# Performance work log

Measured on AMD Instinct MI355X. Metric: run time of the kernel, lower is better.

The kernel has to match this reference:

```python
import jax, jax.numpy as jnp
import numpy as np

# Straight-through sign binarization: forward -> {-1, +1}, backward -> identity
@jax.custom_vjp
def binarize(x):
    return jnp.where(x >= 0, jnp.ones_like(x), -jnp.ones_like(x))

def _bin_fwd(x):
    return binarize(x), None

def _bin_bwd(res, g):
    return (g,)

binarize.defvjp(_bin_fwd, _bin_bwd)

BATCH = 16384
IN_SIZE = 1025   # must be 2**n + 1
HIDDEN = 1025    # must be 2**n + 1

def setup_inputs() -> dict:
    key = jax.random.key(0)
    k0, k1, k2, k3 = jax.random.split(key, 4)
    # weight init scale per reset_parameters: sqrt(1.5/(in+out)) uniform
    s = float(np.sqrt(1.5 / (IN_SIZE + HIDDEN)))
    return {
        "x": jax.random.normal(k0, (BATCH, IN_SIZE), dtype=jnp.float32),
        "W0": jax.random.uniform(k1, (HIDDEN, IN_SIZE), jnp.float32, -s, s),
        "W1": jax.random.uniform(k2, (HIDDEN, HIDDEN), jnp.float32, -s, s),
        "W2": jax.random.uniform(k3, (1, HIDDEN), jnp.float32, -s, s),
    }

def reference(x, W0, W1, W2):
    # x: [B, IN_SIZE]; weights stored [out, in] (nn.Linear convention), no bias
    h = x.reshape(-1, IN_SIZE)
    for W in (W0, W1, W2):
        lin = h @ binarize(W).T          # float GEMM against +/-1 weights
        h = binarize(lin)                # sign activation
    # num_classes == 2 path: to_boolean maps {-1,+1} -> {0,1}, then squeeze
    out = (h + 1.0) * 0.5
    return out.squeeze(-1)               # [B]
```

## Files before the change

kernel.cpp:

```cpp
#include <hip/hip_runtime.h>
#include <cstdint>

typedef unsigned long long u64;
typedef unsigned short ushort_t;
typedef __attribute__((ext_vector_type(8))) short short8;
typedef __attribute__((ext_vector_type(4))) float f32x4;

#define B_TOTAL 16384
#define K_DIM   1025
#define O_DIM   1025
#define NWORDS  17
#define NKT     34
#define NFRAG   72
#define A_BYTES 8192
#define B_BYTES 73728
#define STEP_BYTES (A_BYTES + B_BYTES)
#define FLAG_CAP 4096

__device__ __forceinline__ ushort_t f2bf_rne(float f) {
  unsigned u = __float_as_uint(f);
  return (ushort_t)((u + 0x7fffu + ((u >> 16) & 1u)) >> 16);
}

__device__ __forceinline__ void gload16(const ushort_t* g, char* l) {
  __builtin_amdgcn_global_load_lds(
      (const __attribute__((address_space(1))) void*)g,
      (__attribute__((address_space(3))) void*)l, 16, 0, 0);
}

__global__ __launch_bounds__(256) void pack_all_kernel(const float* __restrict__ W0,
                                                       const float* __restrict__ W1,
                                                       const float* __restrict__ W2,
                                                       u64* __restrict__ w0b,
                                                       u64* __restrict__ w1b,
                                                       u64* __restrict__ w2b) {
  __shared__ unsigned char by[136];
  const int row = blockIdx.x, t = threadIdx.x;
  const float* src; u64* dst; int o;
  if (row < O_DIM)           { src = W0; dst = w0b; o = row; }
  else if (row < 2 * O_DIM)  { src = W1; dst = w1b; o = row - O_DIM; }
  else                       { src = W2; dst = w2b; o = 0; }
  if (t < 136) {
    const float* wr = src + (size_t)o * K_DIM;
    unsigned m = 0;
#pragma unroll
    for (int j = 0; j < 8; ++j) {
      int k = t * 8 + j;
      bool pos = (k < K_DIM) ? (wr[k] >= 0.0f) : true;
      m |= (unsigned)pos << j;
    }
    by[t] = (unsigned char)m;
  }
  __syncthreads();
  if (t < NWORDS) {
    u64 word = 0;
#pragma unroll
    for (int q = 0; q < 8; ++q) word |= (u64)by[t * 8 + q] << (8 * q);
    dst[(size_t)o * NWORDS + t] = word;
  }
}

__global__ __launch_bounds__(256) void prep_sbf_kernel(const float* __restrict__ w0,
                                                       ushort_t* __restrict__ sbf) {
  const int t = threadIdx.x;
  const int f = blockIdx.x * 4 + (t >> 6);
  const int lane = t & 63;
  const int kt = f / NFRAG, nf = f % NFRAG;
  const int o = nf * 16 + (lane & 15);
  const int kbase = kt * 32 + (lane >> 4) * 8;
  short8 sv;
#pragma unroll
  for (int j = 0; j < 8; ++j) {
    int k = kbase + j;
    short v = 0;
    if (o < O_DIM && k < K_DIM)
      v = (short)((w0[(size_t)o * K_DIM + k] >= 0.0f) ? 0x3F80 : 0xBF80);
    sv[j] = v;
  }
  *(short8*)&sbf[(size_t)f * 512 + lane * 8] = sv;
}

__global__ __launch_bounds__(256) void prep_xf_kernel(const float* __restrict__ x,
                                                      ushort_t* __restrict__ xf,
                                                      float* __restrict__ errb) {
  const int p = blockIdx.x, t = threadIdx.x;
  const int mf = t >> 6, lane = t & 63;
  const int lr = lane & 15, lg = lane >> 4;
  const int brow = p * 64 + mf * 16 + lr;
  const float* xr = x + (size_t)brow * K_DIM;
  float s = 0.0f;
  for (int kt = 0; kt < NKT; ++kt) {
    const int kbase = kt * 32 + lg * 8;
    float v[8];
    if (kbase + 8 <= K_DIM) {
      float4 a = *(const float4*)(xr + kbase);
      float4 b = *(const float4*)(xr + kbase + 4);
      v[0]=a.x; v[1]=a.y; v[2]=a.z; v[3]=a.w; v[4]=b.x; v[5]=b.y; v[6]=b.z; v[7]=b.w;
    } else {
#pragma unroll
      for (int j = 0; j < 8; ++j) v[j] = (kbase + j < K_DIM) ? xr[kbase + j] : 0.0f;
    }
    short8 hi, lo;
#pragma unroll
    for (int j = 0; j < 8; ++j) {
      s += fabsf(v[j]);
      ushort_t h = f2bf_rne(v[j]);
      float hf = __uint_as_float((unsigned)h << 16);
      ushort_t l = f2bf_rne(v[j] - hf);
      hi[j] = (short)h; lo[j] = (short)l;
    }
    size_t base = ((size_t)(p * NKT + kt) * 8 + mf) * 512 + lane * 8;
    *(short8*)&xf[base] = hi;
    *(short8*)&xf[base + 4 * 512] = lo;
  }
  s += __shfl_xor(s, 16, 64);
  s += __shfl_xor(s, 32, 64);
  if (lg == 0) errb[brow] = s * (1.02f / 65536.0f) + 0.125f;
}

__global__ __launch_bounds__(512, 2) void l1_fused_kernel(
    const ushort_t* __restrict__ xf, const ushort_t* __restrict__ sbf,
    const float* __restrict__ errb, const float* __restrict__ x,
    const u64* __restrict__ w0b, const u64* __restrict__ w1b,
    const u64* __restrict__ w2b, float* __restrict__ out) {
  extern __shared__ char smem[];
  const int p = blockIdx.x;
  const int t = threadIdx.x;
  const int wave = t >> 6, lane = t & 63;
  const int lr = lane & 15, lg = lane >> 4;
  const int b0 = p * 64;
  const int obase = wave * 144;

  const ushort_t* gA = xf + (size_t)p * NKT * (A_BYTES / 2);

  f32x4 acc[4][9];
#pragma unroll
  for (int mf = 0; mf < 4; ++mf)
#pragma unroll
    for (int nfl = 0; nfl < 9; ++nfl)
#pragma unroll
      for (int c = 0; c < 4; ++c) acc[mf][nfl][c] = 0.0f;

#define STAGE(BUFI, KT)                                                        \
  {                                                                            \
    char* dbuf = smem + (BUFI) * STEP_BYTES;                                   \
    _Pragma("unroll")                                                          \
    for (int i = 0; i < 10; ++i) {                                             \
      int s = wave * 10 + i;                                                   \
      const ushort_t* g = (s < 8)                                              \
          ? gA + (KT) * (A_BYTES / 2) + s * 512 + lane * 8                     \
          : sbf + (size_t)(KT) * (B_BYTES / 2) + (s - 8) * 512 + lane * 8;     \
      gload16(g, dbuf + s * 1024);                                             \
    }                                                                          \
  }

  STAGE(0, 0);
  __syncthreads();
  int cur = 0;
  for (int kt = 0; kt < NKT; ++kt) {
    if (kt + 1 < NKT) STAGE(cur ^ 1, kt + 1);
    const ushort_t* A = (const ushort_t*)(smem + cur * STEP_BYTES);
    const ushort_t* Bf = A + A_BYTES / 2;
    short8 ah[4], al[4];
#pragma unroll
    for (int mf = 0; mf < 4; ++mf) {
      ah[mf] = *(const short8*)&A[mf * 512 + lane * 8];
      al[mf] = *(const short8*)&A[(4 + mf) * 512 + lane * 8];
    }
#pragma unroll
    for (int nfl = 0; nfl < 9; ++nfl) {
      short8 bv = *(const short8*)&Bf[(wave * 9 + nfl) * 512 + lane * 8];
#pragma unroll
      for (int mf = 0; mf < 4; ++mf) {
        acc[mf][nfl] = __builtin_amdgcn_mfma_f32_16x16x32_bf16(ah[mf], bv, acc[mf][nfl], 0, 0, 0);
        acc[mf][nfl] = __builtin_amdgcn_mfma_f32_16x16x32_bf16(al[mf], bv, acc[mf][nfl], 0, 0, 0);
      }
    }
    __syncthreads();
    cur ^= 1;
  }
#undef STAGE

  unsigned char* bits = (unsigned char*)smem;
  u64*      hs   = (u64*)(smem + 73728);
  u64*      h2   = (u64*)(smem + 82432);
  unsigned* list = (unsigned*)(smem + 91136);
  unsigned* lcnt = (unsigned*)(smem + 107520);
  unsigned* hsw  = (unsigned*)hs;

  if (t == 0) *lcnt = 0;
  __syncthreads();

  float eb[4][4];
#pragma unroll
  for (int mf = 0; mf < 4; ++mf)
#pragma unroll
    for (int rg = 0; rg < 4; ++rg) eb[mf][rg] = errb[b0 + mf * 16 + lg * 4 + rg];

#pragma unroll
  for (int mf = 0; mf < 4; ++mf)
#pragma unroll
    for (int nfl = 0; nfl < 9; ++nfl)
#pragma unroll
      for (int rg = 0; rg < 4; ++rg) {
        int bl = mf * 16 + lg * 4 + rg;
        int o  = obase + nfl * 16 + lr;
        float lin = acc[mf][nfl][rg];
        unsigned abit = (lin >= 0.0f) ? 1u : 0u;
        bits[bl * 1152 + o] = (unsigned char)abit;
        if ((o < O_DIM) && (fabsf(lin) <= eb[mf][rg])) {
          unsigned idx = atomicAdd(lcnt, 1u);
          if (idx < FLAG_CAP)
            list[idx] = ((unsigned)bl << 12) | ((unsigned)o << 1) | abit;
        }
      }
  __syncthreads();

  for (int task = t; task < 64 * NWORDS; task += 512) {
    int row = task / NWORDS, w = task % NWORDS;
    u64 word = 0;
#pragma unroll
    for (int q = 0; q < 8; ++q) {
      u64 v = *(const u64*)&bits[row * 1152 + w * 64 + q * 8];
#pragma unroll
      for (int m = 0; m < 8; ++m)
        word |= ((v >> (8 * m)) & 1ull) << (q * 8 + m);
    }
    int rem = O_DIM - w * 64;
    if (rem < 64) word |= (~0ull << rem);
    hs[row * NWORDS + w] = word;
  }
  __syncthreads();

  {
    unsigned n = *lcnt; if (n > FLAG_CAP) n = FLAG_CAP;
    for (unsigned i = t; i < n; i += 512) {
      unsigned en = list[i];
      int bl = (int)(en >> 12), o = (int)((en >> 1) & 0x7ffu);
      unsigned abit = en & 1u;
      const float* xr = x + (size_t)(b0 + bl) * K_DIM;
      const u64* wr = w0b + (size_t)o * NWORDS;
      float a = 0.0f;
      for (int j = 0; j < 16; ++j) {
        u64 wd = wr[j];
#pragma unroll
        for (int m = 0; m < 64; ++m) {
          float v = xr[j * 64 + m];
          unsigned neg = ((unsigned)(wd >> m) & 1u) ^ 1u;
          a += __uint_as_float(__float_as_uint(v) ^ (neg << 31));
        }
      }
      {
        u64 wd = wr[16];
        float v = xr[1024];
        unsigned neg = ((unsigned)wd & 1u) ^ 1u;
        a += __uint_as_float(__float_as_uint(v) ^ (neg << 31));
      }
      unsigned nb = (a >= 0.0f) ? 1u : 0u;
      if (nb != abit)
        atomicXor(&hsw[bl * 34 + (o >> 5)], 1u << (o & 31));
    }
  }
  __syncthreads();

  {
    const int wv = t >> 6, l = t & 63;
    for (int oc = wv; oc < NWORDS; oc += 8) {
      int o = oc * 64 + l;
      bool valid = (o < O_DIM);
      int orow = valid ? o : (O_DIM - 1);
      u64 wb[NWORDS];
#pragma unroll
      for (int j = 0; j < NWORDS; ++j) wb[j] = w1b[(size_t)orow * NWORDS + j];
      for (int b = 0; b < 64; b += 2) {
        int p0 = 0, p1 = 0;
#pragma unroll
        for (int j = 0; j < NWORDS; ++j) {
          p0 += __popcll(hs[(b + 0) * NWORDS + j] ^ wb[j]);
          p1 += __popcll(hs[(b + 1) * NWORDS + j] ^ wb[j]);
        }
        u64 m0 = __ballot(valid ? (K_DIM - 2 * p0 >= 0) : true);
        u64 m1 = __ballot(valid ? (K_DIM - 2 * p1 >= 0) : true);
        if (l == 0) h2[(b + 0) * NWORDS + oc] = m0;
        if (l == 1) h2[(b + 1) * NWORDS + oc] = m1;
      }
    }
  }
  __syncthreads();

  if (t < 64) {
    int pc = 0;
#pragma unroll
    for (int j = 0; j < NWORDS; ++j) pc += __popcll(h2[t * NWORDS + j] ^ w2b[j]);
    out[b0 + t] = ((K_DIM - 2 * pc) >= 0) ? 1.0f : 0.0f;
  }
}

extern "C" void kernel_launch(void* const* d_in, const int* in_sizes, int n_in,
                              void* d_out, int out_size, void* d_ws, size_t ws_size,
                              hipStream_t stream) {
  const float* x  = (const float*)d_in[0];
  const float* W0 = (const float*)d_in[1];
  const float* W1 = (const float*)d_in[2];
  const float* W2 = (const float*)d_in[3];
  float* out = (float*)d_out;

  char* ws = (char*)d_ws;
  u64*      w0b  = (u64*)(ws);
  u64*      w1b  = (u64*)(ws + 139776);
  u64*      w2b  = (u64*)(ws + 279552);
  float*    errb = (float*)(ws + 279808);
  ushort_t* sbf  = (ushort_t*)(ws + 345344);
  ushort_t* xf   = (ushort_t*)(ws + 2852096);

  static bool attr_set = false;
  if (!attr_set) {
    hipFuncSetAttribute((const void*)l1_fused_kernel,
                        hipFuncAttributeMaxDynamicSharedMemorySize, 2 * STEP_BYTES);
    attr_set = true;
  }

  pack_all_kernel<<<2 * O_DIM + 1, 256, 0, stream>>>(W0, W1, W2, w0b, w1b, w2b);
  prep_sbf_kernel<<<NKT * NFRAG / 4, 256, 0, stream>>>(W0, sbf);
  prep_xf_kernel<<<B_TOTAL / 64, 256, 0, stream>>>(x, xf, errb);
  l1_fused_kernel<<<B_TOTAL / 64, 512, 2 * STEP_BYTES, stream>>>(
      xf, sbf, errb, x, w0b, w1b, w2b, out);
}
```

Before: 180.7 us.

## Merge prep kernels and split layers 2-3 into a separate finely-gridded kernel

Merges the three preprocessing kernels into one launch using block-index ranges. Moves the layer-2/3 popcount GEMM out of the fused layer-1 kernel into a new kernel over 8-row batches, with W1 bits stored transposed so lane loads are coalesced. Layer-1 writes its binarized activations to global memory for the new kernel. This trades an extra launch and a global round trip of the hidden bits for better parallelism in the popcount stage and a shorter tail in the heavy MFMA kernel.

```diff
diff --git a/kernel.cpp b/kernel.cpp
--- a/kernel.cpp
+++ b/kernel.cpp
@@ -16,6 +16,7 @@
 #define B_BYTES 73728
 #define STEP_BYTES (A_BYTES + B_BYTES)
 #define FLAG_CAP 4096
+#define L23_ROWS 8
 
 __device__ __forceinline__ ushort_t f2bf_rne(float f) {
   unsigned u = __float_as_uint(f);
@@ -28,18 +29,76 @@
       (__attribute__((address_space(3))) void*)l, 16, 0, 0);
 }
 
-__global__ __launch_bounds__(256) void pack_all_kernel(const float* __restrict__ W0,
-                                                       const float* __restrict__ W1,
-                                                       const float* __restrict__ W2,
-                                                       u64* __restrict__ w0b,
-                                                       u64* __restrict__ w1b,
-                                                       u64* __restrict__ w2b) {
+__global__ __launch_bounds__(256) void prep_kernel(
+    const float* __restrict__ x, const float* __restrict__ W0,
+    const float* __restrict__ W1, const float* __restrict__ W2,
+    ushort_t* __restrict__ xf, float* __restrict__ errb,
+    ushort_t* __restrict__ sbf, u64* __restrict__ w0b,
+    u64* __restrict__ w1t, u64* __restrict__ w2b) {
   __shared__ unsigned char by[136];
-  const int row = blockIdx.x, t = threadIdx.x;
-  const float* src; u64* dst; int o;
-  if (row < O_DIM)           { src = W0; dst = w0b; o = row; }
-  else if (row < 2 * O_DIM)  { src = W1; dst = w1b; o = row - O_DIM; }
-  else                       { src = W2; dst = w2b; o = 0; }
+  const int bid = blockIdx.x, t = threadIdx.x;
+
+  if (bid < 256) {
+    const int p = bid;
+    const int mf = t >> 6, lane = t & 63;
+    const int lr = lane & 15, lg = lane >> 4;
+    const int brow = p * 64 + mf * 16 + lr;
+    const float* xr = x + (size_t)brow * K_DIM;
+    float s = 0.0f;
+    for (int kt = 0; kt < NKT; ++kt) {
+      const int kbase = kt * 32 + lg * 8;
+      float v[8];
+      if (kbase + 8 <= K_DIM) {
+        float4 a = *(const float4*)(xr + kbase);
+        float4 b = *(const float4*)(xr + kbase + 4);
+        v[0]=a.x; v[1]=a.y; v[2]=a.z; v[3]=a.w; v[4]=b.x; v[5]=b.y; v[6]=b.z; v[7]=b.w;
+      } else {
+#pragma unroll
+        for (int j = 0; j < 8; ++j) v[j] = (kbase + j < K_DIM) ? xr[kbase + j] : 0.0f;
+      }
+      short8 hi, lo;
+#pragma unroll
+      for (int j = 0; j < 8; ++j) {
+        s += fabsf(v[j]);
+        ushort_t h = f2bf_rne(v[j]);
+        float hf = __uint_as_float((unsigned)h << 16);
+        ushort_t l = f2bf_rne(v[j] - hf);
+        hi[j] = (short)h; lo[j] = (short)l;
+      }
+      size_t base = ((size_t)(p * NKT + kt) * 8 + mf) * 512 + lane * 8;
+      *(short8*)&xf[base] = hi;
+      *(short8*)&xf[base + 4 * 512] = lo;
+    }
+    s += __shfl_xor(s, 16, 64);
+    s += __shfl_xor(s, 32, 64);
+    if (lg == 0) errb[brow] = s * (1.02f / 65536.0f) + 0.125f;
+    return;
+  }
+
+  if (bid < 868) {
+    const int f = (bid - 256) * 4 + (t >> 6);
+    const int lane = t & 63;
+    const int kt = f / NFRAG, nf = f % NFRAG;
+    const int o = nf * 16 + (lane & 15);
+    const int kbase = kt * 32 + (lane >> 4) * 8;
+    short8 sv;
+#pragma unroll
+    for (int j = 0; j < 8; ++j) {
+      int k = kbase + j;
+      short v = 0;
+      if (o < O_DIM && k < K_DIM)
+        v = (short)((W0[(size_t)o * K_DIM + k] >= 0.0f) ? 0x3F80 : 0xBF80);
+      sv[j] = v;
+    }
+    *(short8*)&sbf[(size_t)f * 512 + lane * 8] = sv;
+    return;
+  }
+
+  const int row = bid - 868;
+  const float* src; int o;
+  if (row < O_DIM)          { src = W0; o = row; }
+  else if (row < 2 * O_DIM) { src = W1; o = row - O_DIM; }
+  else                      { src = W2; o = 0; }
   if (t < 136) {
     const float* wr = src + (size_t)o * K_DIM;
     unsigned m = 0;
@@ -56,73 +115,16 @@
     u64 word = 0;
 #pragma unroll
     for (int q = 0; q < 8; ++q) word |= (u64)by[t * 8 + q] << (8 * q);
-    dst[(size_t)o * NWORDS + t] = word;
-  }
-}
-
-__global__ __launch_bounds__(256) void prep_sbf_kernel(const float* __restrict__ w0,
-                                                       ushort_t* __restrict__ sbf) {
-  const int t = threadIdx.x;
-  const int f = blockIdx.x * 4 + (t >> 6);
-  const int lane = t & 63;
-  const int kt = f / NFRAG, nf = f % NFRAG;
-  const int o = nf * 16 + (lane & 15);
-  const int kbase = kt * 32 + (lane >> 4) * 8;
-  short8 sv;
-#pragma unroll
-  for (int j = 0; j < 8; ++j) {
-    int k = kbase + j;
-    short v = 0;
-    if (o < O_DIM && k < K_DIM)
-      v = (short)((w0[(size_t)o * K_DIM + k] >= 0.0f) ? 0x3F80 : 0xBF80);
-    sv[j] = v;
-  }
-  *(short8*)&sbf[(size_t)f * 512 + lane * 8] = sv;
-}
-
-__global__ __launch_bounds__(256) void prep_xf_kernel(const float* __restrict__ x,
-                                                      ushort_t* __restrict__ xf,
-                                                      float* __restrict__ errb) {
-  const int p = blockIdx.x, t = threadIdx.x;
-  const int mf = t >> 6, lane = t & 63;
-  const int lr = lane & 15, lg = lane >> 4;
-  const int brow = p * 64 + mf * 16 + lr;
-  const float* xr = x + (size_t)brow * K_DIM;
-  float s = 0.0f;
-  for (int kt = 0; kt < NKT; ++kt) {
-    const int kbase = kt * 32 + lg * 8;
-    float v[8];
-    if (kbase + 8 <= K_DIM) {
-      float4 a = *(const float4*)(xr + kbase);
-      float4 b = *(const float4*)(xr + kbase + 4);
-      v[0]=a.x; v[1]=a.y; v[2]=a.z; v[3]=a.w; v[4]=b.x; v[5]=b.y; v[6]=b.z; v[7]=b.w;
-    } else {
-#pragma unroll
-      for (int j = 0; j < 8; ++j) v[j] = (kbase + j < K_DIM) ? xr[kbase + j] : 0.0f;
-    }
-    short8 hi, lo;
-#pragma unroll
-    for (int j = 0; j < 8; ++j) {
-      s += fabsf(v[j]);
-      ushort_t h = f2bf_rne(v[j]);
-      float hf = __uint_as_float((unsigned)h << 16);
-      ushort_t l = f2bf_rne(v[j] - hf);
-      hi[j] = (short)h; lo[j] = (short)l;
-    }
-    size_t base = ((size_t)(p * NKT + kt) * 8 + mf) * 512 + lane * 8;
-    *(short8*)&xf[base] = hi;
-    *(short8*)&xf[base + 4 * 512] = lo;
-  }
-  s += __shfl_xor(s, 16, 64);
-  s += __shfl_xor(s, 32, 64);
-  if (lg == 0) errb[brow] = s * (1.02f / 65536.0f) + 0.125f;
+    if (row < O_DIM)          w0b[(size_t)o * NWORDS + t] = word;
+    else if (row < 2 * O_DIM) w1t[(size_t)t * O_DIM + o] = word;
+    else                      w2b[t] = word;
+  }
 }
 
 __global__ __launch_bounds__(512, 2) void l1_fused_kernel(
     const ushort_t* __restrict__ xf, const ushort_t* __restrict__ sbf,
     const float* __restrict__ errb, const float* __restrict__ x,
-    const u64* __restrict__ w0b, const u64* __restrict__ w1b,
-    const u64* __restrict__ w2b, float* __restrict__ out) {
+    const u64* __restrict__ w0b, u64* __restrict__ h1b) {
   extern __shared__ char smem[];
   const int p = blockIdx.x;
   const int t = threadIdx.x;
@@ -183,9 +185,8 @@
 
   unsigned char* bits = (unsigned char*)smem;
   u64*      hs   = (u64*)(smem + 73728);
-  u64*      h2   = (u64*)(smem + 82432);
-  unsigned* list = (unsigned*)(smem + 91136);
-  unsigned* lcnt = (unsigned*)(smem + 107520);
+  unsigned* list = (unsigned*)(smem + 82432);
+  unsigned* lcnt = (unsigned*)(smem + 98816);
   unsigned* hsw  = (unsigned*)hs;
 
   if (t == 0) *lcnt = 0;
@@ -263,36 +264,49 @@
   }
   __syncthreads();
 
-  {
-    const int wv = t >> 6, l = t & 63;
-    for (int oc = wv; oc < NWORDS; oc += 8) {
-      int o = oc * 64 + l;
-      bool valid = (o < O_DIM);
-      int orow = valid ? o : (O_DIM - 1);
-      u64 wb[NWORDS];
-#pragma unroll
-      for (int j = 0; j < NWORDS; ++j) wb[j] = w1b[(size_t)orow * NWORDS + j];
-      for (int b = 0; b < 64; b += 2) {
-        int p0 = 0, p1 = 0;
-#pragma unroll
-        for (int j = 0; j < NWORDS; ++j) {
-          p0 += __popcll(hs[(b + 0) * NWORDS + j] ^ wb[j]);
-          p1 += __popcll(hs[(b + 1) * NWORDS + j] ^ wb[j]);
-        }
-        u64 m0 = __ballot(valid ? (K_DIM - 2 * p0 >= 0) : true);
-        u64 m1 = __ballot(valid ? (K_DIM - 2 * p1 >= 0) : true);
-        if (l == 0) h2[(b + 0) * NWORDS + oc] = m0;
-        if (l == 1) h2[(b + 1) * NWORDS + oc] = m1;
-      }
-    }
-  }
-  __syncthreads();
-
-  if (t < 64) {
+  for (int task = t; task < 64 * NWORDS; task += 512)
+    h1b[(size_t)b0 * NWORDS + task] = hs[task];
+}
+
+__global__ __launch_bounds__(256) void l2l3_kernel(const u64* __restrict__ h1b,
+                                                   const u64* __restrict__ w1t,
+                                                   const u64* __restrict__ w2b,
+                                                   float* __restrict__ out) {
+  __shared__ u64 hs[L23_ROWS][NWORDS];
+  __shared__ u64 h2[L23_ROWS][NWORDS];
+  const int bt = blockIdx.x;
+  const int t = threadIdx.x;
+  if (t < L23_ROWS * NWORDS)
+    hs[t / NWORDS][t % NWORDS] = h1b[(size_t)bt * L23_ROWS * NWORDS + t];
+  __syncthreads();
+
+  const int w = t >> 6, l = t & 63;
+  for (int oc = w; oc < NWORDS; oc += 4) {
+    int o = oc * 64 + l;
+    bool valid = (o < O_DIM);
+    int orow = valid ? o : (O_DIM - 1);
+    u64 wb[NWORDS];
+#pragma unroll
+    for (int j = 0; j < NWORDS; ++j) wb[j] = w1t[(size_t)j * O_DIM + orow];
+    for (int b = 0; b < L23_ROWS; b += 2) {
+      int p0 = 0, p1 = 0;
+#pragma unroll
+      for (int j = 0; j < NWORDS; ++j) {
+        p0 += __popcll(hs[b + 0][j] ^ wb[j]);
+        p1 += __popcll(hs[b + 1][j] ^ wb[j]);
+      }
+      u64 m0 = __ballot(valid ? (K_DIM - 2 * p0 >= 0) : true);
+      u64 m1 = __ballot(valid ? (K_DIM - 2 * p1 >= 0) : true);
+      if (l == 0) h2[b + 0][oc] = m0;
+      if (l == 1) h2[b + 1][oc] = m1;
+    }
+  }
+  __syncthreads();
+  if (t < L23_ROWS) {
     int pc = 0;
 #pragma unroll
-    for (int j = 0; j < NWORDS; ++j) pc += __popcll(h2[t * NWORDS + j] ^ w2b[j]);
-    out[b0 + t] = ((K_DIM - 2 * pc) >= 0) ? 1.0f : 0.0f;
+    for (int j = 0; j < NWORDS; ++j) pc += __popcll(h2[t][j] ^ w2b[j]);
+    out[bt * L23_ROWS + t] = ((K_DIM - 2 * pc) >= 0) ? 1.0f : 0.0f;
   }
 }
 
@@ -307,11 +321,12 @@
 
   char* ws = (char*)d_ws;
   u64*      w0b  = (u64*)(ws);
-  u64*      w1b  = (u64*)(ws + 139776);
+  u64*      w1t  = (u64*)(ws + 139776);
   u64*      w2b  = (u64*)(ws + 279552);
   float*    errb = (float*)(ws + 279808);
-  ushort_t* sbf  = (ushort_t*)(ws + 345344);
-  ushort_t* xf   = (ushort_t*)(ws + 2852096);
+  u64*      h1b  = (u64*)(ws + 345344);
+  ushort_t* sbf  = (ushort_t*)(ws + 2573824);
+  ushort_t* xf   = (ushort_t*)(ws + 5080576);
 
   static bool attr_set = false;
   if (!attr_set) {
@@ -320,9 +335,9 @@
     attr_set = true;
   }
 
-  pack_all_kernel<<<2 * O_DIM + 1, 256, 0, stream>>>(W0, W1, W2, w0b, w1b, w2b);
-  prep_sbf_kernel<<<NKT * NFRAG / 4, 256, 0, stream>>>(W0, sbf);
-  prep_xf_kernel<<<B_TOTAL / 64, 256, 0, stream>>>(x, xf, errb);
+  prep_kernel<<<256 + 612 + 2051, 256, 0, stream>>>(
+      x, W0, W1, W2, xf, errb, sbf, w0b, w1t, w2b);
   l1_fused_kernel<<<B_TOTAL / 64, 512, 2 * STEP_BYTES, stream>>>(
-      xf, sbf, errb, x, w0b, w1b, w2b, out);
-}
+      xf, sbf, errb, x, w0b, h1b);
+  l2l3_kernel<<<B_TOTAL / L23_ROWS, 256, 0, stream>>>(h1b, w1t, w2b, out);
+}
```

Result: slower. 205.1 us (+13.5%).

## Split binary layers 2-3 out of fused layer-1 kernel into separate wide-grid kernel

Applied to the files above, without the earlier changes.

Moves the popcount-based layer 2 and layer 3 computation out of the big layer-1 MFMA kernel into a new kernel that processes 16 rows per block across 1024 blocks. Layer-1 activations are written as packed bits to a global buffer. This is meant to stop the heavy 512-thread, 2-block-per-CU kernel from running a low-parallelism tail phase in which each wave reloads W1 rows. The cost is an extra launch, a global round trip for the hidden bits, and more total W1 reloads, since each small block reloads all of W1.

```diff
diff --git a/kernel.cpp b/kernel.cpp
--- a/kernel.cpp
+++ b/kernel.cpp
@@ -16,6 +16,7 @@
 #define B_BYTES 73728
 #define STEP_BYTES (A_BYTES + B_BYTES)
 #define FLAG_CAP 4096
+#define L23_ROWS 16
 
 __device__ __forceinline__ ushort_t f2bf_rne(float f) {
   unsigned u = __float_as_uint(f);
@@ -121,8 +122,7 @@
 __global__ __launch_bounds__(512, 2) void l1_fused_kernel(
     const ushort_t* __restrict__ xf, const ushort_t* __restrict__ sbf,
     const float* __restrict__ errb, const float* __restrict__ x,
-    const u64* __restrict__ w0b, const u64* __restrict__ w1b,
-    const u64* __restrict__ w2b, float* __restrict__ out) {
+    const u64* __restrict__ w0b, u64* __restrict__ h1b) {
   extern __shared__ char smem[];
   const int p = blockIdx.x;
   const int t = threadIdx.x;
@@ -183,9 +183,8 @@
 
   unsigned char* bits = (unsigned char*)smem;
   u64*      hs   = (u64*)(smem + 73728);
-  u64*      h2   = (u64*)(smem + 82432);
-  unsigned* list = (unsigned*)(smem + 91136);
-  unsigned* lcnt = (unsigned*)(smem + 107520);
+  unsigned* list = (unsigned*)(smem + 82432);
+  unsigned* lcnt = (unsigned*)(smem + 98816);
   unsigned* hsw  = (unsigned*)hs;
 
   if (t == 0) *lcnt = 0;
@@ -263,36 +262,49 @@
   }
   __syncthreads();
 
-  {
-    const int wv = t >> 6, l = t & 63;
-    for (int oc = wv; oc < NWORDS; oc += 8) {
-      int o = oc * 64 + l;
-      bool valid = (o < O_DIM);
-      int orow = valid ? o : (O_DIM - 1);
-      u64 wb[NWORDS];
-#pragma unroll
-      for (int j = 0; j < NWORDS; ++j) wb[j] = w1b[(size_t)orow * NWORDS + j];
-      for (int b = 0; b < 64; b += 2) {
-        int p0 = 0, p1 = 0;
-#pragma unroll
-        for (int j = 0; j < NWORDS; ++j) {
-          p0 += __popcll(hs[(b + 0) * NWORDS + j] ^ wb[j]);
-          p1 += __popcll(hs[(b + 1) * NWORDS + j] ^ wb[j]);
-        }
-        u64 m0 = __ballot(valid ? (K_DIM - 2 * p0 >= 0) : true);
-        u64 m1 = __ballot(valid ? (K_DIM - 2 * p1 >= 0) : true);
-        if (l == 0) h2[(b + 0) * NWORDS + oc] = m0;
-        if (l == 1) h2[(b + 1) * NWORDS + oc] = m1;
-      }
-    }
-  }
-  __syncthreads();
-
-  if (t < 64) {
-    int pc = 0;
-#pragma unroll
-    for (int j = 0; j < NWORDS; ++j) pc += __popcll(h2[t * NWORDS + j] ^ w2b[j]);
-    out[b0 + t] = ((K_DIM - 2 * pc) >= 0) ? 1.0f : 0.0f;
+  for (int task = t; task < 64 * NWORDS; task += 512)
+    h1b[(size_t)b0 * NWORDS + task] = hs[task];
+}
+
+__global__ __launch_bounds__(256) void l2l3_kernel(const u64* __restrict__ h1b,
+                                                   const u64* __restrict__ w1b,
+                                                   const u64* __restrict__ w2b,
+                                                   float* __restrict__ out) {
+  __shared__ u64 hs[L23_ROWS][NWORDS];
+  __shared__ u64 h2[L23_ROWS][NWORDS];
+  const int bt = blockIdx.x;
+  const int t = threadIdx.x;
+  for (int i = t; i < L23_ROWS * NWORDS; i += 256)
+    hs[i / NWORDS][i % NWORDS] = h1b[(size_t)(bt * L23_ROWS + i / NWORDS) * NWORDS + i % NWORDS];
+  __syncthreads();
+
+  const int w = t >> 6, l = t & 63;
+  for (int oc = w; oc < NWORDS; oc += 4) {
+    int o = oc * 64 + l;
+    bool valid = (o < O_DIM);
+    int orow = valid ? o : (O_DIM - 1);
+    u64 wb[NWORDS];
+#pragma unroll
+    for (int j = 0; j < NWORDS; ++j) wb[j] = w1b[(size_t)orow * NWORDS + j];
+    for (int b = 0; b < L23_ROWS; b += 2) {
+      int p0 = 0, p1 = 0;
+#pragma unroll
+      for (int j = 0; j < NWORDS; ++j) {
+        p0 += __popcll(hs[b + 0][j] ^ wb[j]);
+        p1 += __popcll(hs[b + 1][j] ^ wb[j]);
+      }
+      u64 m0 = __ballot(valid ? (K_DIM - 2 * p0 >= 0) : true);
+      u64 m1 = __ballot(valid ? (K_DIM - 2 * p1 >= 0) : true);
+      if (l == 0) h2[b + 0][oc] = m0;
+      if (l == 1) h2[b + 1][oc] = m1;
+    }
+  }
+  __syncthreads();
+  if (t < L23_ROWS) {
+    int p = 0;
+#pragma unroll
+    for (int j = 0; j < NWORDS; ++j) p += __popcll(h2[t][j] ^ w2b[j]);
+    out[bt * L23_ROWS + t] = ((K_DIM - 2 * p) >= 0) ? 1.0f : 0.0f;
   }
 }
 
@@ -310,8 +322,9 @@
   u64*      w1b  = (u64*)(ws + 139776);
   u64*      w2b  = (u64*)(ws + 279552);
   float*    errb = (float*)(ws + 279808);
-  ushort_t* sbf  = (ushort_t*)(ws + 345344);
-  ushort_t* xf   = (ushort_t*)(ws + 2852096);
+  u64*      h1b  = (u64*)(ws + 345344);
+  ushort_t* sbf  = (ushort_t*)(ws + 2573824);
+  ushort_t* xf   = (ushort_t*)(ws + 5080576);
 
   static bool attr_set = false;
   if (!attr_set) {
@@ -324,5 +337,6 @@
   prep_sbf_kernel<<<NKT * NFRAG / 4, 256, 0, stream>>>(W0, sbf);
   prep_xf_kernel<<<B_TOTAL / 64, 256, 0, stream>>>(x, xf, errb);
   l1_fused_kernel<<<B_TOTAL / 64, 512, 2 * STEP_BYTES, stream>>>(
-      xf, sbf, errb, x, w0b, w1b, w2b, out);
-}
+      xf, sbf, errb, x, w0b, h1b);
+  l2l3_kernel<<<B_TOTAL / L23_ROWS, 256, 0, stream>>>(h1b, w1b, w2b, out);
+}
```

Result: faster. 175.5 us (-2.9%).
